# Kernel optimization log

Measured on AMD Instinct MI355X. Metric: run time of the kernel, lower is better.

## Reference

```python
import jax, jax.numpy as jnp
import numpy as np

B = 16        # graphs per batch
NPG = 4096    # nodes per graph
N = B * NPG
EPG = 32768   # edges per graph
E = B * EPG
F_NODE, F_EDGE, G, H, A = 8, 4, 16, 128, 10


def setup_inputs() -> dict:
    key = jax.random.key(0)
    ks = jax.random.split(key, 32)
    x = jax.random.normal(ks[0], (N, F_NODE), jnp.float32)
    # random intra-graph edges, offset into the batched node id space
    src = jax.random.randint(ks[1], (B, EPG), 0, NPG)
    dst = jax.random.randint(ks[2], (B, EPG), 0, NPG)
    off = (jnp.arange(B) * NPG)[:, None]
    edge_index = jnp.stack([(src + off).reshape(-1), (dst + off).reshape(-1)]).astype(jnp.int64)
    edge_attr = jax.random.normal(ks[3], (E, F_EDGE), jnp.float32)
    global_state = jax.random.normal(ks[4], (B, G), jnp.float32)
    current_pipe_nodes = jax.random.randint(ks[5], (B, 2), 0, NPG).astype(jnp.int64)

    def w(k, shape):
        fan_in = shape[0] if len(shape) > 1 else shape[0]
        return jax.random.normal(k, shape, jnp.float32) * (1.0 / np.sqrt(fan_in))

    return dict(
        x=x, edge_index=edge_index, edge_attr=edge_attr,
        global_state=global_state, current_pipe_nodes=current_pipe_nodes,
        W_l1=w(ks[6], (F_NODE, H)), W_r1=w(ks[7], (F_NODE, H)), W_e1=w(ks[8], (F_EDGE, H)),
        att1=w(ks[9], (H,)), b1=jnp.zeros((H,), jnp.float32),
        W_l2=w(ks[10], (H, H)), W_r2=w(ks[11], (H, H)), W_e2=w(ks[12], (F_EDGE, H)),
        att2=w(ks[13], (H,)), b2=jnp.zeros((H,), jnp.float32),
        W_c=w(ks[14], (H + 2 * H + G, 256)), b_c=jnp.zeros((256,), jnp.float32),
        W_a1=w(ks[15], (256, 128)), b_a1=jnp.zeros((128,), jnp.float32),
        W_a2=w(ks[16], (128, A)), b_a2=jnp.zeros((A,), jnp.float32),
        W_v1=w(ks[17], (256, 128)), b_v1=jnp.zeros((128,), jnp.float32),
        W_v2=w(ks[18], (128, 1)), b_v2=jnp.zeros((1,), jnp.float32),
    )


def add_self_loops(edge_index, edge_attr, n):
    # PyG default: add_self_loops=True, fill_value='mean' -> loop attr is the
    # mean of incoming edge_attr per node (zeros if none).
    dst = edge_index[1]
    deg = jax.ops.segment_sum(jnp.ones(dst.shape, jnp.float32), dst, num_segments=n)
    loop_attr = jax.ops.segment_sum(edge_attr, dst, num_segments=n) / jnp.maximum(deg, 1.0)[:, None]
    loops = jnp.tile(jnp.arange(n, dtype=edge_index.dtype)[None, :], (2, 1))
    ei = jnp.concatenate([edge_index, loops], axis=1)
    ea = jnp.concatenate([edge_attr, loop_attr], axis=0)
    return ei, ea


def gatv2(x, ei, ea, Wl, Wr, We, att, bias, n):
    # GATv2Conv (heads=1): score = att . leaky_relu(Wl x_j + Wr x_i + We e_ij)
    # message = alpha_ij * (Wl x_j); segment softmax over incoming edges of i.
    src, dst = ei[0], ei[1]
    xl = x @ Wl                                   # [N,H]
    xr = x @ Wr                                   # [N,H]
    m = xl[src] + xr[dst] + ea @ We               # [E,H]
    s = jax.nn.leaky_relu(m, 0.2) @ att           # [E]
    smax = jax.ops.segment_max(s, dst, num_segments=n)
    ealpha = jnp.exp(s - smax[dst])
    denom = jax.ops.segment_sum(ealpha, dst, num_segments=n)
    alpha = ealpha / denom[dst]
    out = jax.ops.segment_sum(alpha[:, None] * xl[src], dst, num_segments=n)
    return out + bias


def reference(x, edge_index, edge_attr, global_state, current_pipe_nodes,
              W_l1, W_r1, W_e1, att1, b1,
              W_l2, W_r2, W_e2, att2, b2,
              W_c, b_c, W_a1, b_a1, W_a2, b_a2, W_v1, b_v1, W_v2, b_v2):
    ei, ea = add_self_loops(edge_index, edge_attr, N)
    h = jax.nn.relu(gatv2(x, ei, ea, W_l1, W_r1, W_e1, att1, b1, N))
    h = gatv2(h, ei, ea, W_l2, W_r2, W_e2, att2, b2, N)
    # global_mean_pool: graphs are contiguous equal-size blocks
    graph_emb = h.reshape(B, NPG, H).mean(axis=1)                       # [B,H]
    abs_idx = current_pipe_nodes + (jnp.arange(B) * NPG)[:, None]       # [B,2]
    pipe_emb = h[abs_idx.reshape(-1)].reshape(B, 2 * H)                 # [B,2H]
    comb = jnp.concatenate([graph_emb, pipe_emb, global_state], axis=1)
    feat = jax.nn.relu(comb @ W_c + b_c)
    logits = jax.nn.relu(feat @ W_a1 + b_a1) @ W_a2 + b_a2              # [B,A]
    value = jax.nn.relu(feat @ W_v1 + b_v1) @ W_v2 + b_v2               # [B,1]
    return jnp.concatenate([logits, value], axis=1)                     # [B,A+1]
```

## Files before the change

### kernel.cpp

```cpp
#include <hip/hip_runtime.h>
#include <math.h>

#define NN   65536
#define NPG  4096
#define NB   16
#define NE   524288
#define EPG  32768
#define SB   8
#define NH   128
#define FN   8
#define FE   4
#define NG   16
#define NA   10
#define NFRAG 2048
#define L1B  512

typedef __attribute__((ext_vector_type(8))) short bf16x8;
typedef __attribute__((ext_vector_type(4))) float f32x4;

static __device__ __forceinline__ short bf16rne(float f) {
    unsigned u = __builtin_bit_cast(unsigned, f);
    u += 0x7FFFu + ((u >> 16) & 1u);
    return (short)(u >> 16);
}

__global__ __launch_bounds__(1024) void csr_lin1_kernel(
        const int* __restrict__ ei,
        int* __restrict__ offs, int2* __restrict__ csr,
        const float* __restrict__ x,
        const float* __restrict__ Wl, const float* __restrict__ Wr,
        const float* __restrict__ Wl2, const float* __restrict__ Wr2,
        bf16x8* __restrict__ wbf,
        float* __restrict__ xl, float* __restrict__ xr) {
    int bid = blockIdx.x;
    int t = threadIdx.x;
    if (bid < NB * SB) {
        __shared__ int htot[NPG];
        __shared__ int hpre[NPG];
        __shared__ int psum[1024];
        int g = bid >> 3, sb = bid & 7;
        for (int i = t; i < NPG; i += 1024) { htot[i] = 0; hpre[i] = 0; }
        __syncthreads();
        const int* dstp = ei + NE + g * EPG;
        for (int s = 0; s < SB; ++s) {
            bool pre = s < sb;
            const int* dc = dstp + s * (EPG / SB);
            for (int i = t; i < EPG / SB; i += 1024) {
                int dl = dc[i] - g * NPG;
                atomicAdd(&htot[dl], 1);
                if (pre) atomicAdd(&hpre[dl], 1);
            }
        }
        __syncthreads();
        int base4 = t * 4;
        int loc[4];
        int run = 0;
#pragma unroll
        for (int i = 0; i < 4; ++i) { loc[i] = run; run += htot[base4 + i]; }
        psum[t] = run;
        __syncthreads();
        for (int s = 1; s < 1024; s <<= 1) {
            int add = (t >= s) ? psum[t - s] : 0;
            __syncthreads();
            psum[t] += add;
            __syncthreads();
        }
        int prefix = (t == 0) ? 0 : psum[t - 1];
        int ebase = g * EPG;
#pragma unroll
        for (int i = 0; i < 4; ++i) {
            int nl = base4 + i;
            int off = ebase + prefix + loc[i];
            hpre[nl] += off;
            if (sb == 0) offs[g * NPG + nl] = off;
        }
        if (sb == 0 && g == NB - 1 && t == 0) offs[NN] = NE;
        __syncthreads();
        int e0 = g * EPG + sb * (EPG / SB);
#pragma unroll
        for (int i = 0; i < (EPG / SB) / 1024; ++i) {
            int e = e0 + i * 1024 + t;
            int dst = ei[NE + e];
            int src = ei[e];
            int pos = atomicAdd(&hpre[dst - g * NPG], 1);
            csr[pos] = make_int2(src, e);
        }
    } else if (bid < NB * SB + 2) {
        int sel = bid - NB * SB;
        const float* W = sel ? Wr2 : Wl2;
#pragma unroll
        for (int q = 0; q < 2; ++q) {
            int f = t * 2 + q;
            int lane = f & 63;
            int kgct = f >> 6;
            int kg = kgct & 3, ct = kgct >> 2;
            int kbase = kg * 32 + (lane >> 4) * 8;
            int c = ct * 16 + (lane & 15);
            bf16x8 v;
#pragma unroll
            for (int j = 0; j < 8; ++j)
                v[j] = bf16rne(W[(kbase + j) * NH + c]);
            wbf[sel * NFRAG + f] = v;
        }
    } else {
        int lb = bid - NB * SB - 2;
        int k = t & 127;
        int oct = t >> 7;
        float wl[FN], wr[FN];
#pragma unroll
        for (int j = 0; j < FN; ++j) {
            wl[j] = Wl[j * NH + k];
            wr[j] = Wr[j * NH + k];
        }
        int nbase = lb * 128 + oct * 16;
        for (int i = 0; i < 16; ++i) {
            int n = nbase + i;
            float4 xa = *(const float4*)&x[(size_t)n * FN];
            float4 xb = *(const float4*)&x[(size_t)n * FN + 4];
            float al = xa.x * wl[0] + xa.y * wl[1] + xa.z * wl[2] + xa.w * wl[3]
                     + xb.x * wl[4] + xb.y * wl[5] + xb.z * wl[6] + xb.w * wl[7];
            float ar = xa.x * wr[0] + xa.y * wr[1] + xa.z * wr[2] + xa.w * wr[3]
                     + xb.x * wr[4] + xb.y * wr[5] + xb.z * wr[6] + xb.w * wr[7];
            xl[(size_t)n * NH + k] = al;
            xr[(size_t)n * NH + k] = ar;
        }
    }
}

__global__ __launch_bounds__(256) void gat_gather_kernel(
        const float4* __restrict__ xl, const float4* __restrict__ xr,
        const float4* __restrict__ ea,
        const int2* __restrict__ csr, const int* __restrict__ offs,
        const float* __restrict__ We, const float* __restrict__ att,
        const float* __restrict__ bias,
        unsigned short* __restrict__ hbf_out,
        float4* __restrict__ lattr_w, const float4* __restrict__ lattr_r,
        float4* __restrict__ gpart, float4* __restrict__ pipe,
        const int* __restrict__ cpn, int do_relu) {
    __shared__ float4 red[8][32];
    int grp = threadIdx.x >> 5;
    int lane = threadIdx.x & 31;
    int bid = blockIdx.x;
    int xcd = bid & 7, slot = bid >> 3;
    int g = xcd + ((slot >> 9) << 3);
    int blk = slot & 511;
    int node = g * NPG + blk * 8 + grp;

    float4 xr4 = xr[node * 32 + lane];
    float4 att4 = ((const float4*)att)[lane];
    const float4* We4 = (const float4*)We;
    float4 we0 = We4[lane];
    float4 we1 = We4[32 + lane];
    float4 we2 = We4[64 + lane];
    float4 we3 = We4[96 + lane];

    int beg = offs[node], end = offs[node + 1];
    float l = 0.f;
    float4 acc = make_float4(0.f, 0.f, 0.f, 0.f);
    float4 easum = make_float4(0.f, 0.f, 0.f, 0.f);
    bool have_lattr = (lattr_r != nullptr);
    if (beg < end) {
        int last = end - 1;
        int2 se0 = csr[beg];
        int p1 = (beg + 1 <= last) ? beg + 1 : last;
        int2 se1 = csr[p1];
        float4 xl0 = xl[se0.x * 32 + lane];
        float4 a0 = ea[se0.y];
        for (int p = beg; p < end; ++p) {
            int p2 = (p + 2 <= last) ? p + 2 : last;
            int2 se2 = csr[p2];
            float4 xl1 = xl[se1.x * 32 + lane];
            float4 a1 = ea[se1.y];
            if (!have_lattr) {
                easum.x += a0.x; easum.y += a0.y; easum.z += a0.z; easum.w += a0.w;
            }
            float tx = xl0.x + xr4.x + a0.x * we0.x + a0.y * we1.x + a0.z * we2.x + a0.w * we3.x;
            float ty = xl0.y + xr4.y + a0.x * we0.y + a0.y * we1.y + a0.z * we2.y + a0.w * we3.y;
            float tz = xl0.z + xr4.z + a0.x * we0.z + a0.y * we1.z + a0.z * we2.z + a0.w * we3.z;
            float tw = xl0.w + xr4.w + a0.x * we0.w + a0.y * we1.w + a0.z * we2.w + a0.w * we3.w;
            tx = tx > 0.f ? tx : 0.2f * tx;
            ty = ty > 0.f ? ty : 0.2f * ty;
            tz = tz > 0.f ? tz : 0.2f * tz;
            tw = tw > 0.f ? tw : 0.2f * tw;
            float s = tx * att4.x + ty * att4.y + tz * att4.z + tw * att4.w;
#pragma unroll
            for (int o = 16; o >= 1; o >>= 1) s += __shfl_xor(s, o);
            float w = __expf(s);
            l += w;
            acc.x += w * xl0.x;
            acc.y += w * xl0.y;
            acc.z += w * xl0.z;
            acc.w += w * xl0.w;
            se1 = se2; xl0 = xl1; a0 = a1;
        }
    }
    {
        float ax, ay, az, aw;
        if (have_lattr) {
            float4 la = lattr_r[node];
            ax = la.x; ay = la.y; az = la.z; aw = la.w;
        } else {
            int deg = end - beg;
            float invd = 1.0f / (float)(deg > 0 ? deg : 1);
            ax = easum.x * invd; ay = easum.y * invd;
            az = easum.z * invd; aw = easum.w * invd;
            if (lane == 0) lattr_w[node] = make_float4(ax, ay, az, aw);
        }
        float4 xl4 = xl[node * 32 + lane];
        float tx = xl4.x + xr4.x + ax * we0.x + ay * we1.x + az * we2.x + aw * we3.x;
        float ty = xl4.y + xr4.y + ax * we0.y + ay * we1.y + az * we2.y + aw * we3.y;
        float tz = xl4.z + xr4.z + ax * we0.z + ay * we1.z + az * we2.z + aw * we3.z;
        float tw = xl4.w + xr4.w + ax * we0.w + ay * we1.w + az * we2.w + aw * we3.w;
        tx = tx > 0.f ? tx : 0.2f * tx;
        ty = ty > 0.f ? ty : 0.2f * ty;
        tz = tz > 0.f ? tz : 0.2f * tz;
        tw = tw > 0.f ? tw : 0.2f * tw;
        float s = tx * att4.x + ty * att4.y + tz * att4.z + tw * att4.w;
#pragma unroll
        for (int o = 16; o >= 1; o >>= 1) s += __shfl_xor(s, o);
        float w = __expf(s);
        l += w;
        acc.x += w * xl4.x;
        acc.y += w * xl4.y;
        acc.z += w * xl4.z;
        acc.w += w * xl4.w;
    }
    float inv = 1.0f / l;
    float4 b4 = ((const float4*)bias)[lane];
    float4 o4;
    o4.x = acc.x * inv + b4.x;
    o4.y = acc.y * inv + b4.y;
    o4.z = acc.z * inv + b4.z;
    o4.w = acc.w * inv + b4.w;
    if (do_relu) {
        o4.x = fmaxf(o4.x, 0.f); o4.y = fmaxf(o4.y, 0.f);
        o4.z = fmaxf(o4.z, 0.f); o4.w = fmaxf(o4.w, 0.f);
    }
    if (hbf_out != nullptr) {
        int rt = node >> 4, m = node & 15;
        int kg = lane >> 3, qd = (lane & 7) >> 1, j0 = (lane & 1) * 4;
        ushort4 v;
        v.x = (unsigned short)bf16rne(o4.x);
        v.y = (unsigned short)bf16rne(o4.y);
        v.z = (unsigned short)bf16rne(o4.z);
        v.w = (unsigned short)bf16rne(o4.w);
        *(ushort4*)&hbf_out[(size_t)(((rt * 4 + kg) * 64 + qd * 16 + m)) * 8 + j0] = v;
    } else {
        int nl = node - g * NPG;
        if (nl == cpn[g * 2 + 0]) pipe[(g * 2 + 0) * 32 + lane] = o4;
        if (nl == cpn[g * 2 + 1]) pipe[(g * 2 + 1) * 32 + lane] = o4;
    }

    if (gpart != nullptr) {
        red[grp][lane] = o4;
        __syncthreads();
        if (grp < 4) {
            float4 o = red[grp + 4][lane];
            red[grp][lane] = make_float4(red[grp][lane].x + o.x, red[grp][lane].y + o.y,
                                         red[grp][lane].z + o.z, red[grp][lane].w + o.w);
        }
        __syncthreads();
        if (grp < 2) {
            float4 o = red[grp + 2][lane];
            red[grp][lane] = make_float4(red[grp][lane].x + o.x, red[grp][lane].y + o.y,
                                         red[grp][lane].z + o.z, red[grp][lane].w + o.w);
        }
        __syncthreads();
        if (grp == 0) {
            float4 a = red[0][lane], b = red[1][lane];
            gpart[(g * 512 + blk) * 32 + lane] =
                make_float4(a.x + b.x, a.y + b.y, a.z + b.z, a.w + b.w);
        }
    }
}

__global__ __launch_bounds__(256) void lin2_mfma_kernel(
        const bf16x8* __restrict__ hbf, const bf16x8* __restrict__ wbf,
        float* __restrict__ xl, float* __restrict__ xr) {
    const bf16x8* Bf = wbf + (size_t)blockIdx.y * NFRAG;
    float* C = blockIdx.y ? xr : xl;
    int t = threadIdx.x;
    int wv = t >> 6, lane = t & 63;
    int rt = blockIdx.x * 4 + wv;
    int row0 = rt * 16;
    int m = lane & 15, qd = lane >> 4;
    bf16x8 afrag[4];
#pragma unroll
    for (int kg = 0; kg < 4; ++kg)
        afrag[kg] = hbf[(size_t)(rt * 4 + kg) * 64 + lane];
#pragma unroll
    for (int ct = 0; ct < 8; ++ct) {
        f32x4 acc = {0.f, 0.f, 0.f, 0.f};
#pragma unroll
        for (int kg = 0; kg < 4; ++kg) {
            bf16x8 b = Bf[((ct << 2) | kg) * 64 + lane];
            acc = __builtin_amdgcn_mfma_f32_16x16x32_bf16(afrag[kg], b, acc, 0, 0, 0);
        }
        int col = ct * 16 + m;
#pragma unroll
        for (int r = 0; r < 4; ++r)
            C[(size_t)(row0 + qd * 4 + r) * NH + col] = acc[r];
    }
}

__global__ __launch_bounds__(1024) void head_kernel(
        const float* __restrict__ gpart, const float* __restrict__ pipe,
        const float* __restrict__ gstate,
        const float* __restrict__ Wc, const float* __restrict__ bc,
        const float* __restrict__ Wa1, const float* __restrict__ ba1,
        const float* __restrict__ Wa2, const float* __restrict__ ba2,
        const float* __restrict__ Wv1, const float* __restrict__ bv1,
        const float* __restrict__ Wv2, const float* __restrict__ bv2,
        float* __restrict__ out) {
    int b = blockIdx.x, t = threadIdx.x;
    __shared__ float comb[400];
    __shared__ float part[4][256];
    __shared__ float pp[8][128];
    __shared__ float feat[256];
    __shared__ float hid[256];
    {
        int d = t & 127, p = t >> 7;
        const float* gp = gpart + (size_t)b * 512 * NH + d;
        float s = 0.f;
        int c0 = p * 64;
        for (int c = c0; c < c0 + 64; ++c) s += gp[c * NH];
        pp[p][d] = s;
    }
    if (t >= 128 && t < 384) comb[t] = pipe[(size_t)b * 2 * NH + (t - 128)];
    else if (t >= 384 && t < 400) comb[t] = gstate[b * NG + (t - 384)];
    __syncthreads();
    if (t < 128) {
        float s = pp[0][t] + pp[1][t] + pp[2][t] + pp[3][t]
                + pp[4][t] + pp[5][t] + pp[6][t] + pp[7][t];
        comb[t] = s * (1.0f / NPG);
    }
    __syncthreads();
    {
        int col = t & 255, p = t >> 8;
        float a = 0.f;
        int j0 = p * 100;
        for (int j = j0; j < j0 + 100; ++j) a += comb[j] * Wc[j * 256 + col];
        part[p][col] = a;
    }
    __syncthreads();
    if (t < 256)
        feat[t] = fmaxf(bc[t] + part[0][t] + part[1][t] + part[2][t] + part[3][t], 0.f);
    __syncthreads();
    {
        int col = t & 255, p = t >> 8;
        const float* W = (col < 128) ? Wa1 : Wv1;
        int cc = col & 127;
        float a = 0.f;
        int j0 = p * 64;
        for (int j = j0; j < j0 + 64; ++j) a += feat[j] * W[j * 128 + cc];
        part[p][col] = a;
    }
    __syncthreads();
    if (t < 256) {
        float bias = (t < 128) ? ba1[t] : bv1[t - 128];
        hid[t] = fmaxf(bias + part[0][t] + part[1][t] + part[2][t] + part[3][t], 0.f);
    }
    __syncthreads();
    if (t < NA) {
        float a2 = ba2[t];
        for (int j = 0; j < NH; ++j) a2 += hid[j] * Wa2[j * NA + t];
        out[b * 11 + t] = a2;
    } else if (t == NA) {
        float a2 = bv2[0];
        for (int j = 0; j < NH; ++j) a2 += hid[128 + j] * Wv2[j];
        out[b * 11 + 10] = a2;
    }
}

extern "C" void kernel_launch(void* const* d_in, const int* in_sizes, int n_in,
                              void* d_out, int out_size, void* d_ws, size_t ws_size,
                              hipStream_t stream) {
    const float* x      = (const float*)d_in[0];
    const int*   ei     = (const int*)d_in[1];
    const float* ea     = (const float*)d_in[2];
    const float* gstate = (const float*)d_in[3];
    const int*   cpn    = (const int*)d_in[4];
    const float* Wl1 = (const float*)d_in[5];
    const float* Wr1 = (const float*)d_in[6];
    const float* We1 = (const float*)d_in[7];
    const float* att1= (const float*)d_in[8];
    const float* b1  = (const float*)d_in[9];
    const float* Wl2 = (const float*)d_in[10];
    const float* Wr2 = (const float*)d_in[11];
    const float* We2 = (const float*)d_in[12];
    const float* att2= (const float*)d_in[13];
    const float* b2  = (const float*)d_in[14];
    const float* Wc  = (const float*)d_in[15];
    const float* bc  = (const float*)d_in[16];
    const float* Wa1 = (const float*)d_in[17];
    const float* ba1 = (const float*)d_in[18];
    const float* Wa2 = (const float*)d_in[19];
    const float* ba2 = (const float*)d_in[20];
    const float* Wv1 = (const float*)d_in[21];
    const float* bv1 = (const float*)d_in[22];
    const float* Wv2 = (const float*)d_in[23];
    const float* bv2 = (const float*)d_in[24];

    char* ws = (char*)d_ws;
    size_t o = 0;
    float* xl     = (float*)(ws + o); o += (size_t)NN * NH * 4;
    float* xr     = (float*)(ws + o); o += (size_t)NN * NH * 4;
    unsigned short* hbf = (unsigned short*)(ws + o); o += (size_t)NN * NH * 2;
    float* lattr  = (float*)(ws + o); o += (size_t)NN * 16;
    float* gpart  = (float*)(ws + o); o += (size_t)NB * 512 * NH * 4;
    float* pipe   = (float*)(ws + o); o += (size_t)NB * 2 * NH * 4;
    int*   offs   = (int*)(ws + o);   o += (((size_t)(NN + 1) * 4 + 255) & ~(size_t)255);
    int2*  csr    = (int2*)(ws + o);  o += (size_t)NE * 8;
    bf16x8* wbf   = (bf16x8*)(ws + o); o += (size_t)2 * NFRAG * 16;
    (void)o; (void)ws_size; (void)in_sizes; (void)n_in; (void)out_size;

    csr_lin1_kernel<<<NB * SB + 2 + L1B, 1024, 0, stream>>>(ei, offs, csr,
        x, Wl1, Wr1, Wl2, Wr2, wbf, xl, xr);
    gat_gather_kernel<<<NN / 8, 256, 0, stream>>>((const float4*)xl, (const float4*)xr,
        (const float4*)ea, csr, offs, We1, att1, b1, hbf,
        (float4*)lattr, nullptr, nullptr, nullptr, cpn, 1);
    lin2_mfma_kernel<<<dim3(NN / 64, 2), 256, 0, stream>>>((const bf16x8*)hbf, wbf, xl, xr);
    gat_gather_kernel<<<NN / 8, 256, 0, stream>>>((const float4*)xl, (const float4*)xr,
        (const float4*)ea, csr, offs, We2, att2, b2, nullptr,
        nullptr, (const float4*)lattr, (float4*)gpart, (float4*)pipe, cpn, 0);
    head_kernel<<<NB, 1024, 0, stream>>>(gpart, pipe, gstate, Wc, bc, Wa1, ba1, Wa2, ba2,
                                         Wv1, bv1, Wv2, bv2, (float*)d_out);
}
```

Measured before the change: 271.4 us.

## Bin nodes by in-degree and gather in degree-sorted order

```diff
diff --git a/kernel.cpp b/kernel.cpp
--- a/kernel.cpp
+++ b/kernel.cpp
@@ -14,6 +14,7 @@
 #define NA   10
 #define NFRAG 2048
 #define L1B  512
+#define NBIN 32
 
 typedef __attribute__((ext_vector_type(8))) short bf16x8;
 typedef __attribute__((ext_vector_type(4))) float f32x4;
@@ -26,7 +27,7 @@
 
 __global__ __launch_bounds__(1024) void csr_lin1_kernel(
         const int* __restrict__ ei,
-        int* __restrict__ offs, int2* __restrict__ csr,
+        int* __restrict__ offs, int2* __restrict__ csr, int* __restrict__ perm,
         const float* __restrict__ x,
         const float* __restrict__ Wl, const float* __restrict__ Wr,
         const float* __restrict__ Wl2, const float* __restrict__ Wr2,
@@ -38,8 +39,10 @@
         __shared__ int htot[NPG];
         __shared__ int hpre[NPG];
         __shared__ int psum[1024];
+        __shared__ int bins[NBIN];
         int g = bid >> 3, sb = bid & 7;
         for (int i = t; i < NPG; i += 1024) { htot[i] = 0; hpre[i] = 0; }
+        if (t < NBIN) bins[t] = 0;
         __syncthreads();
         const int* dstp = ei + NE + g * EPG;
         for (int s = 0; s < SB; ++s) {
@@ -53,10 +56,21 @@
         }
         __syncthreads();
         int base4 = t * 4;
-        int loc[4];
+        int loc[4], dg[4];
         int run = 0;
 #pragma unroll
-        for (int i = 0; i < 4; ++i) { loc[i] = run; run += htot[base4 + i]; }
+        for (int i = 0; i < 4; ++i) {
+            dg[i] = htot[base4 + i];
+            loc[i] = run;
+            run += dg[i];
+        }
+        if (sb == 0) {
+#pragma unroll
+            for (int i = 0; i < 4; ++i) {
+                int bi = dg[i] < NBIN ? dg[i] : NBIN - 1;
+                atomicAdd(&bins[bi], 1);
+            }
+        }
         psum[t] = run;
         __syncthreads();
         for (int s = 1; s < 1024; s <<= 1) {
@@ -75,7 +89,21 @@
             if (sb == 0) offs[g * NPG + nl] = off;
         }
         if (sb == 0 && g == NB - 1 && t == 0) offs[NN] = NE;
-        __syncthreads();
+        if (sb == 0 && t == 0) {
+            int acc = 0;
+#pragma unroll
+            for (int i = 0; i < NBIN; ++i) { int v = bins[i]; bins[i] = acc; acc += v; }
+        }
+        __syncthreads();
+        if (sb == 0) {
+#pragma unroll
+            for (int i = 0; i < 4; ++i) {
+                int nl = base4 + i;
+                int bi = dg[i] < NBIN ? dg[i] : NBIN - 1;
+                int r = atomicAdd(&bins[bi], 1);
+                perm[g * NPG + r] = nl;
+            }
+        }
         int e0 = g * EPG + sb * (EPG / SB);
 #pragma unroll
         for (int i = 0; i < (EPG / SB) / 1024; ++i) {
@@ -131,6 +159,7 @@
         const float4* __restrict__ xl, const float4* __restrict__ xr,
         const float4* __restrict__ ea,
         const int2* __restrict__ csr, const int* __restrict__ offs,
+        const int* __restrict__ perm,
         const float* __restrict__ We, const float* __restrict__ att,
         const float* __restrict__ bias,
         unsigned short* __restrict__ hbf_out,
@@ -144,7 +173,7 @@
     int xcd = bid & 7, slot = bid >> 3;
     int g = xcd + ((slot >> 9) << 3);
     int blk = slot & 511;
-    int node = g * NPG + blk * 8 + grp;
+    int node = g * NPG + perm[g * NPG + blk * 8 + grp];
 
     float4 xr4 = xr[node * 32 + lane];
     float4 att4 = ((const float4*)att)[lane];
@@ -410,18 +439,19 @@
     float* gpart  = (float*)(ws + o); o += (size_t)NB * 512 * NH * 4;
     float* pipe   = (float*)(ws + o); o += (size_t)NB * 2 * NH * 4;
     int*   offs   = (int*)(ws + o);   o += (((size_t)(NN + 1) * 4 + 255) & ~(size_t)255);
+    int*   perm   = (int*)(ws + o);   o += (size_t)NN * 4;
     int2*  csr    = (int2*)(ws + o);  o += (size_t)NE * 8;
     bf16x8* wbf   = (bf16x8*)(ws + o); o += (size_t)2 * NFRAG * 16;
     (void)o; (void)ws_size; (void)in_sizes; (void)n_in; (void)out_size;
 
-    csr_lin1_kernel<<<NB * SB + 2 + L1B, 1024, 0, stream>>>(ei, offs, csr,
+    csr_lin1_kernel<<<NB * SB + 2 + L1B, 1024, 0, stream>>>(ei, offs, csr, perm,
         x, Wl1, Wr1, Wl2, Wr2, wbf, xl, xr);
     gat_gather_kernel<<<NN / 8, 256, 0, stream>>>((const float4*)xl, (const float4*)xr,
-        (const float4*)ea, csr, offs, We1, att1, b1, hbf,
+        (const float4*)ea, csr, offs, perm, We1, att1, b1, hbf,
         (float4*)lattr, nullptr, nullptr, nullptr, cpn, 1);
     lin2_mfma_kernel<<<dim3(NN / 64, 2), 256, 0, stream>>>((const bf16x8*)hbf, wbf, xl, xr);
     gat_gather_kernel<<<NN / 8, 256, 0, stream>>>((const float4*)xl, (const float4*)xr,
-        (const float4*)ea, csr, offs, We2, att2, b2, nullptr,
+        (const float4*)ea, csr, offs, perm, We2, att2, b2, nullptr,
         nullptr, (const float4*)lattr, (float4*)gpart, (float4*)pipe, cpn, 0);
     head_kernel<<<NB, 1024, 0, stream>>>(gpart, pipe, gstate, Wc, bc, Wa1, ba1, Wa2, ba2,
                                          Wv1, bv1, Wv2, bv2, (float*)d_out);
```

After: 269.4 us. Within noise of the previous version (-0.7%).
